# Kernel tuning notes

Measured on AMD Instinct MI355X. Metric: run time of the kernel, lower is better.

## Reference

```python
import jax, jax.numpy as jnp
import numpy as np
from jax import lax

N_LAYERS = 10
N_BLOCKS = 3
N_STACK = N_LAYERS * N_BLOCKS  # 30
WIDTH = 512
SKIP_W = 256
CH = 1
QUANT = 256
BOTTLENECK = 16
KSIZE = 3
SCALE = 2 ** (N_LAYERS - 1)  # 512, nearest upsample factor
B, T = 1, 16384
T_EMB = T // SCALE  # 32


def causal_conv(x, w, b, dilation):
    # x: [B,Cin,T], w: [Cout,Cin,K] -> causal dilated conv, output [B,Cout,T]
    k = w.shape[-1]
    pad = (k - 1) * dilation
    y = lax.conv_general_dilated(x, w, window_strides=(1,), padding=[(pad, 0)],
                                 rhs_dilation=(dilation,),
                                 dimension_numbers=('NCH', 'OIH', 'NCH'))
    return y + b[None, :, None]


def conv1x1(x, w, b):
    # x: [B,Cin,T], w: [Cout,Cin]
    return jnp.einsum('oc,bct->bot', w, x) + b[None, :, None]


def setup_inputs() -> dict:
    key = jax.random.key(0)
    ks = jax.random.split(key, 24)
    s = 0.05
    inp = {
        'x': jax.random.normal(ks[0], (B, CH, T), jnp.float32),
        'embedding': jax.random.normal(ks[1], (B, BOTTLENECK, T_EMB), jnp.float32),
        'w_init': jax.random.normal(ks[2], (WIDTH, CH, KSIZE), jnp.float32) * s,
        'b_init': jnp.zeros((WIDTH,), jnp.float32),
        'w_iskip': jax.random.normal(ks[3], (SKIP_W, WIDTH), jnp.float32) * s,
        'b_iskip': jnp.zeros((SKIP_W,), jnp.float32),
        'w_dil': jax.random.normal(ks[4], (N_STACK, 2 * WIDTH, WIDTH, KSIZE), jnp.float32) * s,
        'b_dil': jnp.zeros((N_STACK, 2 * WIDTH), jnp.float32),
        'w_cond': jax.random.normal(ks[5], (N_STACK, 2 * WIDTH, BOTTLENECK), jnp.float32) * s,
        'b_cond': jnp.zeros((N_STACK, 2 * WIDTH), jnp.float32),
        'w_res': jax.random.normal(ks[6], (N_STACK, WIDTH, WIDTH), jnp.float32) * s,
        'b_res': jnp.zeros((N_STACK, WIDTH), jnp.float32),
        'w_skip': jax.random.normal(ks[7], (N_STACK, SKIP_W, WIDTH), jnp.float32) * s,
        'b_skip': jnp.zeros((N_STACK, SKIP_W), jnp.float32),
        'w_fskip': jax.random.normal(ks[8], (SKIP_W, SKIP_W), jnp.float32) * s,
        'b_fskip': jnp.zeros((SKIP_W,), jnp.float32),
        'w_fcond': jax.random.normal(ks[9], (SKIP_W, BOTTLENECK), jnp.float32) * s,
        'b_fcond': jnp.zeros((SKIP_W,), jnp.float32),
        'w_quant': jax.random.normal(ks[10], (QUANT, SKIP_W), jnp.float32) * s,
        'b_quant': jnp.zeros((QUANT,), jnp.float32),
    }
    return inp


def reference(x, embedding, w_init, b_init, w_iskip, b_iskip, w_dil, b_dil,
              w_cond, b_cond, w_res, b_res, w_skip, b_skip,
              w_fskip, b_fskip, w_fcond, b_fcond, w_quant, b_quant):
    # initial causal conv (kernel 3, dilation 1) + initial skip 1x1
    h = causal_conv(x, w_init, b_init, 1)            # [B,WIDTH,T]
    skip = conv1x1(h, w_iskip, b_iskip)              # [B,SKIP_W,T]
    for i in range(N_STACK):
        dilation = 2 ** (i % N_LAYERS)
        cond = conv1x1(embedding, w_cond[i], b_cond[i])      # [B,2W,T_EMB]
        cond_up = jnp.repeat(cond, SCALE, axis=-1)           # nearest upsample -> [B,2W,T]
        dilated = causal_conv(h, w_dil[i], b_dil[i], dilation) + cond_up
        filters = jax.nn.sigmoid(dilated[:, :WIDTH, :])
        gates = jnp.tanh(dilated[:, WIDTH:, :])
        pre = filters * gates
        h = h + conv1x1(pre, w_res[i], b_res[i])
        skip = skip + conv1x1(pre, w_skip[i], b_skip[i])
    skip = conv1x1(jax.nn.relu(skip), w_fskip, b_fskip)
    fcond = jnp.repeat(conv1x1(embedding, w_fcond, b_fcond), SCALE, axis=-1)
    skip = skip + fcond
    return conv1x1(jax.nn.relu(skip), w_quant, b_quant)     # [B,QUANT,T]
```

## Files before the change

### kernel.cpp

```cpp
#include <hip/hip_runtime.h>


typedef _Float16 f16x8 __attribute__((ext_vector_type(8)));
typedef float f32x4 __attribute__((ext_vector_type(4)));

#define NSTACK 30
#define TLEN   16384

typedef __attribute__((address_space(1))) const unsigned int glob_u32;
typedef __attribute__((address_space(3))) unsigned int lds_u32;

__device__ __forceinline__ void gll16(const unsigned short* g, unsigned short* l) {
  __builtin_amdgcn_global_load_lds((glob_u32*)g, (lds_u32*)l, 16, 0, 0);
}

__device__ __forceinline__ unsigned short f2h(float x) {
  union { _Float16 h; unsigned short u; } c;
  c.h = (_Float16)x;
  return c.u;
}
__device__ __forceinline__ unsigned pack2(float a, float b) {
  return (unsigned)f2h(a) | ((unsigned)f2h(b) << 16);
}
__device__ __forceinline__ float uplo(unsigned u){ union{unsigned v;_Float16 h[2];}c; c.v=u; return (float)c.h[0]; }
__device__ __forceinline__ float uphi(unsigned u){ union{unsigned v;_Float16 h[2];}c; c.v=u; return (float)c.h[1]; }
__device__ __forceinline__ f16x8 ldh(const unsigned short* p) {
  return *(const f16x8*)p;
}
__device__ __forceinline__ float sigmoidf_(float x){ return 1.0f/(1.0f+__expf(-x)); }
__device__ __forceinline__ float tanhf_(float x){ return 1.0f - 2.0f/(__expf(2.0f*x)+1.0f); }
#define MFMA16(a,b,c) __builtin_amdgcn_mfma_f32_16x16x32_f16((a),(b),(c),0,0,0)

#define SEG_T  15728640L
#define SEG_R  1966080L
#define SEG_S  983040L
#define SEG_I  32768L
#define SEG_F  16384L
#define SEG_Q  16384L
#define SEG_C  30976L
#define PREP_TOTAL (SEG_T+SEG_R+SEG_S+SEG_I+SEG_F+SEG_Q+SEG_C)

__device__ __forceinline__ void cast4(const float* src, unsigned short* dst, long g){
  f32x4 v = *(const f32x4*)(src + 4*g);
  unsigned int* d = (unsigned int*)(dst + 4*g);
  d[0] = pack2(v[0], v[1]);
  d[1] = pack2(v[2], v[3]);
}

__global__ void prep_kernel(
    const float* __restrict__ w_dil,  unsigned short* __restrict__ A_dil,
    const float* __restrict__ w_res,  unsigned short* __restrict__ Wres_h,
    const float* __restrict__ w_skip, unsigned short* __restrict__ Wskip_h,
    const float* __restrict__ w_iskip,unsigned short* __restrict__ Wiskip_h,
    const float* __restrict__ w_fskip,unsigned short* __restrict__ Wfskip_h,
    const float* __restrict__ w_quant,unsigned short* __restrict__ Wquant_h,
    const float* __restrict__ emb,
    const float* __restrict__ w_cond, const float* __restrict__ b_cond,
    const float* __restrict__ b_dil,
    const float* __restrict__ w_fcond,const float* __restrict__ b_fcond,
    float* __restrict__ cond_all, float* __restrict__ fcond_all) {
  long g = (long)blockIdx.x*256 + threadIdx.x;
  if (g < SEG_T) {
    int c = (int)(g & 511);
    int m = (int)((g >> 9) & 1023);
    int i = (int)(g >> 19);
    const float* s = w_dil + g*3;
    #pragma unroll
    for (int tap=0; tap<3; ++tap)
      A_dil[(((size_t)i*3+tap)*1024 + m)*512 + c] = f2h(s[tap]);
    return;
  }
  g -= SEG_T;
  if (g < SEG_R) { cast4(w_res,  Wres_h,  g); return; }
  g -= SEG_R;
  if (g < SEG_S) { cast4(w_skip, Wskip_h, g); return; }
  g -= SEG_S;
  if (g < SEG_I) { cast4(w_iskip, Wiskip_h, g); return; }
  g -= SEG_I;
  if (g < SEG_F) { cast4(w_fskip, Wfskip_h, g); return; }
  g -= SEG_F;
  if (g < SEG_Q) { cast4(w_quant, Wquant_h, g); return; }
  g -= SEG_Q;
  if (g < NSTACK*1024) {
    int row = (int)g;
    float acc[32];
    float base = b_cond[row] + b_dil[row];
    #pragma unroll
    for (int e=0;e<32;++e) acc[e] = base;
    #pragma unroll
    for (int c=0;c<16;++c) {
      float wv = w_cond[(size_t)row*16 + c];
      #pragma unroll
      for (int e=0;e<32;++e) acc[e] += wv * emb[c*32+e];
    }
    #pragma unroll
    for (int e=0;e<32;++e) cond_all[(size_t)row*32+e] = acc[e];
  } else if (g < NSTACK*1024 + 256) {
    int m = (int)(g - NSTACK*1024);
    float acc[32];
    float base = b_fcond[m];
    #pragma unroll
    for (int c=0;c<16;++c) {
      float wv = w_fcond[(size_t)m*16 + c];
      #pragma unroll
      for (int e=0;e<32;++e) acc[e] = (c==0 ? base : acc[e]) + wv * emb[c*32+e];
    }
    #pragma unroll
    for (int e=0;e<32;++e) fcond_all[(size_t)m*32+e] = acc[e];
  }
}

__global__ __launch_bounds__(512) void hs_kernel(
    const float* __restrict__ x, const float* __restrict__ w_init,
    const float* __restrict__ b_init,
    unsigned short* __restrict__ h_h16,
    const unsigned short* __restrict__ Wiskip,
    const float* __restrict__ b_iskip, unsigned short* __restrict__ skip16) {
  __shared__ unsigned short S[64][520];
  const int tid = threadIdx.x;
  const int tb = blockIdx.x << 6;

  for (int j = tid; j < 64*128; j += 512) {
    int r  = j >> 7;
    int c4 = (j & 127) << 2;
    int t  = tb + r;
    float xm2 = (t>=2)? x[t-2] : 0.f;
    float xm1 = (t>=1)? x[t-1] : 0.f;
    float x0  = x[t];
    float hv[4];
    #pragma unroll
    for (int q=0;q<4;++q) {
      int cc = c4 + q;
      hv[q] = w_init[cc*3+0]*xm2 + w_init[cc*3+1]*xm1 + w_init[cc*3+2]*x0 + b_init[cc];
    }
    unsigned p0 = pack2(hv[0],hv[1]), p1 = pack2(hv[2],hv[3]);
    unsigned int* hb = (unsigned int*)&h_h16[(size_t)t*512 + c4];
    hb[0] = p0; hb[1] = p1;
    unsigned int* sb = (unsigned int*)&S[r][c4];
    sb[0] = p0; sb[1] = p1;
  }
  __syncthreads();

  const int w = tid >> 6, l = tid & 63, lr = l & 15, lc = l >> 4;
  f32x4 acc[2][4];
  #pragma unroll
  for (int mf=0;mf<2;++mf)
    #pragma unroll
    for (int nf=0;nf<4;++nf) acc[mf][nf] = {0.f,0.f,0.f,0.f};
  for (int kc=0;kc<512;kc+=32) {
    f16x8 b[4];
    #pragma unroll
    for (int nf=0;nf<4;++nf)
      b[nf] = ldh(&S[16*nf+lr][kc + lc*8]);
    #pragma unroll
    for (int mf=0;mf<2;++mf) {
      f16x8 a = ldh(&Wiskip[(size_t)(w*32+16*mf+lr)*512 + kc + lc*8]);
      #pragma unroll
      for (int nf=0;nf<4;++nf)
        acc[mf][nf] = MFMA16(a, b[nf], acc[mf][nf]);
    }
  }
  #pragma unroll
  for (int mf=0;mf<2;++mf)
    #pragma unroll
    for (int nf=0;nf<4;++nf) {
      int s0 = w*32+16*mf+4*lc;
      int t  = tb+16*nf+lr;
      unsigned int* pp = (unsigned int*)&skip16[(size_t)t*256+s0];
      pp[0] = pack2(acc[mf][nf][0]+b_iskip[s0+0], acc[mf][nf][1]+b_iskip[s0+1]);
      pp[1] = pack2(acc[mf][nf][2]+b_iskip[s0+2], acc[mf][nf][3]+b_iskip[s0+3]);
    }
}

__global__ __launch_bounds__(512, 4) void dil_kernel(
    const unsigned short* __restrict__ h_in,
    unsigned short* __restrict__ pre,
    const unsigned short* __restrict__ A_dil,
    const float* __restrict__ cond,
    const unsigned short* __restrict__ zerobuf,
    int dilation) {
  __shared__ unsigned short Ab[2][128][32];
  __shared__ unsigned short Bb[2][256][32];
  const int tid = threadIdx.x;
  const int w = tid >> 6, l = tid & 63;
  const int lr = l & 15, lc = l >> 4;
  const int nt = blockIdx.x & 63, mt = blockIdx.x >> 6;
  const int tb = nt << 8;
  const int e  = tb >> 9;
  const int wr = w >> 2, wc = w & 3;

  const int srowA = (w<<4) + (l>>2);
  const int srowB0 = (w<<5) + (l>>2);
  const int schunk = (l & 3) << 3;

  f32x4 fa[2][4], ga[2][4];
  #pragma unroll
  for (int mf=0;mf<2;++mf)
    #pragma unroll
    for (int nf=0;nf<4;++nf) { fa[mf][nf] = {0.f,0.f,0.f,0.f}; ga[mf][nf] = {0.f,0.f,0.f,0.f}; }

  auto stage = [&](int buf, int s){
    const int tap = s >> 4;
    const int kc  = (s & 15) << 5;
    const int shift = (2 - tap) * dilation;
    {
      const int r = srowA;
      const int m = mt*64 + r + ((r>>6)*448);
      gll16(A_dil + (size_t)tap*(1024*512) + (size_t)m*512 + kc + schunk,
            &Ab[buf][(w<<4)][0]);
    }
    #pragma unroll
    for (int j=0;j<2;++j){
      const int r = srowB0 + (j<<4);
      const int t = tb + r - shift;
      const unsigned short* srcB = (t >= 0) ? (h_in + (size_t)t*512 + kc + schunk)
                                            : (zerobuf + schunk);
      gll16(srcB, &Bb[buf][(w<<5)+(j<<4)][0]);
    }
  };

  stage(0, 0);
  for (int s=0; s<48; ++s) {
    const int cur = s & 1;
    __syncthreads();
    if (s+1 < 48) stage(cur^1, s+1);
    f16x8 af[2], ag[2], bf[4];
    #pragma unroll
    for (int mf=0;mf<2;++mf){
      const int row = (wr<<5) + (mf<<4) + lr;
      af[mf] = ldh(&Ab[cur][row][lc<<3]);
      ag[mf] = ldh(&Ab[cur][64+row][lc<<3]);
    }
    #pragma unroll
    for (int nf=0;nf<4;++nf)
      bf[nf] = ldh(&Bb[cur][(wc<<6)+(nf<<4)+lr][lc<<3]);
    #pragma unroll
    for (int mf=0;mf<2;++mf)
      #pragma unroll
      for (int nf=0;nf<4;++nf){
        fa[mf][nf] = MFMA16(af[mf], bf[nf], fa[mf][nf]);
        ga[mf][nf] = MFMA16(ag[mf], bf[nf], ga[mf][nf]);
      }
  }

  #pragma unroll
  for (int mf=0;mf<2;++mf)
    #pragma unroll
    for (int nf=0;nf<4;++nf){
      const int m0 = mt*64 + (wr<<5) + (mf<<4) + (lc<<2);
      const int t  = tb + (wc<<6) + (nf<<4) + lr;
      float pv[4];
      #pragma unroll
      for (int r=0;r<4;++r){
        float f = fa[mf][nf][r] + cond[(size_t)(m0+r)*32 + e];
        float g = ga[mf][nf][r] + cond[(size_t)(m0+r+512)*32 + e];
        pv[r] = sigmoidf_(f) * tanhf_(g);
      }
      unsigned int* pp = (unsigned int*)&pre[(size_t)t*512 + m0];
      pp[0] = pack2(pv[0], pv[1]);
      pp[1] = pack2(pv[2], pv[3]);
    }
}

__global__ __launch_bounds__(512, 4) void ressk_kernel(
    const unsigned short* __restrict__ pre,
    const unsigned short* __restrict__ h_in,
    unsigned short* __restrict__ h_out,
    unsigned short* __restrict__ skip16,
    const unsigned short* __restrict__ Wres,
    const unsigned short* __restrict__ Wskip,
    const float* __restrict__ b_res,
    const float* __restrict__ b_skip) {
  __shared__ unsigned short Ab[2][128][32];
  __shared__ unsigned short Bb[2][256][32];
  const int tid = threadIdx.x;
  const int w = tid >> 6, l = tid & 63;
  const int lr = l & 15, lc = l >> 4;
  const int nt = blockIdx.x & 63, mt = blockIdx.x >> 6;
  const int tb = nt << 8;
  const int wr = w >> 2, wc = w & 3;
  const bool isres = (mt < 4);
  const unsigned short* W = isres ? Wres : Wskip;
  const int mrow0 = (isres ? mt : (mt-4)) * 128;

  const int srowA = (w<<4) + (l>>2);
  const int srowB0 = (w<<5) + (l>>2);
  const int schunk = (l & 3) << 3;

  f32x4 acc[4][4];
  #pragma unroll
  for (int mf=0;mf<4;++mf)
    #pragma unroll
    for (int nf=0;nf<4;++nf) acc[mf][nf] = {0.f,0.f,0.f,0.f};

  auto stage = [&](int buf, int s){
    const int kc = s << 5;
    gll16(W + (size_t)(mrow0 + srowA)*512 + kc + schunk, &Ab[buf][(w<<4)][0]);
    #pragma unroll
    for (int j=0;j<2;++j){
      const int r = srowB0 + (j<<4);
      gll16(pre + (size_t)(tb + r)*512 + kc + schunk, &Bb[buf][(w<<5)+(j<<4)][0]);
    }
  };

  stage(0, 0);
  for (int s=0; s<16; ++s) {
    const int cur = s & 1;
    __syncthreads();
    if (s+1 < 16) stage(cur^1, s+1);
    f16x8 a[4], bf[4];
    #pragma unroll
    for (int mf=0;mf<4;++mf)
      a[mf] = ldh(&Ab[cur][(wr<<6)+(mf<<4)+lr][lc<<3]);
    #pragma unroll
    for (int nf=0;nf<4;++nf)
      bf[nf] = ldh(&Bb[cur][(wc<<6)+(nf<<4)+lr][lc<<3]);
    #pragma unroll
    for (int mf=0;mf<4;++mf)
      #pragma unroll
      for (int nf=0;nf<4;++nf)
        acc[mf][nf] = MFMA16(a[mf], bf[nf], acc[mf][nf]);
  }

  if (isres) {
    #pragma unroll
    for (int mf=0;mf<4;++mf)
      #pragma unroll
      for (int nf=0;nf<4;++nf){
        const int m0 = mrow0 + (wr<<6) + (mf<<4) + (lc<<2);
        const int t  = tb + (wc<<6) + (nf<<4) + lr;
        const unsigned int* hi = (const unsigned int*)&h_in[(size_t)t*512 + m0];
        unsigned int h01 = hi[0], h23 = hi[1];
        float v0 = uplo(h01) + acc[mf][nf][0] + b_res[m0+0];
        float v1 = uphi(h01) + acc[mf][nf][1] + b_res[m0+1];
        float v2 = uplo(h23) + acc[mf][nf][2] + b_res[m0+2];
        float v3 = uphi(h23) + acc[mf][nf][3] + b_res[m0+3];
        unsigned int* hb = (unsigned int*)&h_out[(size_t)t*512 + m0];
        hb[0] = pack2(v0,v1); hb[1] = pack2(v2,v3);
      }
  } else {
    #pragma unroll
    for (int mf=0;mf<4;++mf)
      #pragma unroll
      for (int nf=0;nf<4;++nf){
        const int s0 = mrow0 + (wr<<6) + (mf<<4) + (lc<<2);
        const int t  = tb + (wc<<6) + (nf<<4) + lr;
        unsigned int* sp = (unsigned int*)&skip16[(size_t)t*256 + s0];
        unsigned int s01 = sp[0], s23 = sp[1];
        float v0 = uplo(s01) + acc[mf][nf][0] + b_skip[s0+0];
        float v1 = uphi(s01) + acc[mf][nf][1] + b_skip[s0+1];
        float v2 = uplo(s23) + acc[mf][nf][2] + b_skip[s0+2];
        float v3 = uphi(s23) + acc[mf][nf][3] + b_skip[s0+3];
        sp[0] = pack2(v0,v1); sp[1] = pack2(v2,v3);
      }
  }
}

__global__ __launch_bounds__(512) void final_kernel(
    const unsigned short* __restrict__ skip16, const unsigned short* __restrict__ Wfs,
    const float* __restrict__ b_fskip, const float* __restrict__ fcond,
    const unsigned short* __restrict__ Wq, const float* __restrict__ b_quant,
    float* __restrict__ out) {
  __shared__ unsigned short S1[64][264];
  __shared__ unsigned short S2[64][264];
  int tid=threadIdx.x, w=tid>>6, l=tid&63, lr=l&15, lc=l>>4;
  int tb = blockIdx.x<<6, e = tb>>9;

  for (int j = tid; j < 64*32; j += 512) {
    int r  = j >> 5;
    int c8 = (j & 31) << 3;
    const unsigned int* sp = (const unsigned int*)&skip16[(size_t)(tb+r)*256 + c8];
    unsigned int* dp = (unsigned int*)&S1[r][c8];
    #pragma unroll
    for (int q=0;q<4;++q){
      unsigned int u = sp[q];
      dp[q] = pack2(fmaxf(uplo(u),0.f), fmaxf(uphi(u),0.f));
    }
  }
  __syncthreads();

  f32x4 acc[2][4];
  #pragma unroll
  for (int mf=0;mf<2;++mf)
    #pragma unroll
    for (int nf=0;nf<4;++nf) acc[mf][nf] = {0.f,0.f,0.f,0.f};
  for (int kc=0;kc<256;kc+=32) {
    f16x8 b[4];
    #pragma unroll
    for (int nf=0;nf<4;++nf) b[nf] = ldh(&S1[16*nf+lr][kc + lc*8]);
    #pragma unroll
    for (int mf=0;mf<2;++mf) {
      f16x8 a = ldh(&Wfs[(size_t)(w*32+16*mf+lr)*256 + kc + lc*8]);
      #pragma unroll
      for (int nf=0;nf<4;++nf)
        acc[mf][nf] = MFMA16(a, b[nf], acc[mf][nf]);
    }
  }
  #pragma unroll
  for (int mf=0;mf<2;++mf)
    #pragma unroll
    for (int nf=0;nf<4;++nf) {
      int m0 = w*32+16*mf+4*lc;
      int n  = 16*nf+lr;
      float pv[4];
      #pragma unroll
      for (int r=0;r<4;++r) {
        float v = acc[mf][nf][r] + b_fskip[m0+r] + fcond[(size_t)(m0+r)*32 + e];
        pv[r] = fmaxf(v, 0.f);
      }
      unsigned int* pp = (unsigned int*)&S2[n][m0];
      pp[0] = pack2(pv[0],pv[1]); pp[1] = pack2(pv[2],pv[3]);
    }
  __syncthreads();

  f32x4 acc2[2][4];
  #pragma unroll
  for (int mf=0;mf<2;++mf)
    #pragma unroll
    for (int nf=0;nf<4;++nf) acc2[mf][nf] = {0.f,0.f,0.f,0.f};
  for (int kc=0;kc<256;kc+=32) {
    f16x8 b[4];
    #pragma unroll
    for (int nf=0;nf<4;++nf) b[nf] = ldh(&S2[16*nf+lr][kc + lc*8]);
    #pragma unroll
    for (int mf=0;mf<2;++mf) {
      f16x8 a = ldh(&Wq[(size_t)(w*32+16*mf+lr)*256 + kc + lc*8]);
      #pragma unroll
      for (int nf=0;nf<4;++nf)
        acc2[mf][nf] = MFMA16(a, b[nf], acc2[mf][nf]);
    }
  }
  #pragma unroll
  for (int mf=0;mf<2;++mf)
    #pragma unroll
    for (int nf=0;nf<4;++nf) {
      int q0 = w*32+16*mf+4*lc;
      int t  = tb + 16*nf + lr;
      #pragma unroll
      for (int r=0;r<4;++r)
        out[(size_t)(q0+r)*TLEN + t] = acc2[mf][nf][r] + b_quant[q0+r];
    }
}


extern "C" void kernel_launch(void* const* d_in, const int* in_sizes, int n_in,
                              void* d_out, int out_size, void* d_ws, size_t ws_size,
                              hipStream_t stream) {
  const float* x       = (const float*)d_in[0];
  const float* emb     = (const float*)d_in[1];
  const float* w_init  = (const float*)d_in[2];
  const float* b_init  = (const float*)d_in[3];
  const float* w_iskip = (const float*)d_in[4];
  const float* b_iskip = (const float*)d_in[5];
  const float* w_dil   = (const float*)d_in[6];
  const float* b_dil   = (const float*)d_in[7];
  const float* w_cond  = (const float*)d_in[8];
  const float* b_cond  = (const float*)d_in[9];
  const float* w_res   = (const float*)d_in[10];
  const float* b_res   = (const float*)d_in[11];
  const float* w_skip  = (const float*)d_in[12];
  const float* b_skip  = (const float*)d_in[13];
  const float* w_fskip = (const float*)d_in[14];
  const float* b_fskip = (const float*)d_in[15];
  const float* w_fcond = (const float*)d_in[16];
  const float* b_fcond = (const float*)d_in[17];
  const float* w_quant = (const float*)d_in[18];
  const float* b_quant = (const float*)d_in[19];
  float* out = (float*)d_out;

  char* ws = (char*)d_ws;
  size_t off = 0;
  auto carve = [&](size_t bytes) -> void* {
    void* p = ws + off;
    off += (bytes + 255) & ~(size_t)255;
    return p;
  };
  unsigned short* A_dil     = (unsigned short*)carve((size_t)NSTACK*3*1024*512*2);
  unsigned short* Wres_h    = (unsigned short*)carve((size_t)NSTACK*512*512*2);
  unsigned short* Wskip_h   = (unsigned short*)carve((size_t)NSTACK*256*512*2);
  unsigned short* Wiskip_h  = (unsigned short*)carve((size_t)256*512*2);
  unsigned short* Wfskip_h  = (unsigned short*)carve((size_t)256*256*2);
  unsigned short* Wquant_h  = (unsigned short*)carve((size_t)256*256*2);
  unsigned short* h_h16     = (unsigned short*)carve((size_t)2*TLEN*512*2);
  unsigned short* pre_h16   = (unsigned short*)carve((size_t)TLEN*512*2);
  unsigned short* skip_h16  = (unsigned short*)carve((size_t)TLEN*256*2);
  float*          cond_all  = (float*)carve((size_t)NSTACK*1024*32*4);
  float*          fcond_all = (float*)carve((size_t)256*32*4);
  unsigned short* zerobuf   = (unsigned short*)carve((size_t)512*2);
  if (off > ws_size) return;

  hipMemsetAsync(zerobuf, 0, 512*2, stream);

  prep_kernel<<<(int)(PREP_TOTAL/256), 256, 0, stream>>>(
      w_dil, A_dil, w_res, Wres_h, w_skip, Wskip_h, w_iskip, Wiskip_h,
      w_fskip, Wfskip_h, w_quant, Wquant_h,
      emb, w_cond, b_cond, b_dil, w_fcond, b_fcond, cond_all, fcond_all);

  hs_kernel<<<TLEN/64, 512, 0, stream>>>(
      x, w_init, b_init, h_h16, Wiskip_h, b_iskip, skip_h16);

  const size_t HB = (size_t)TLEN*512;
  for (int i = 0; i < NSTACK; ++i) {
    int d = 1 << (i % 10);
    const unsigned short* h_in = h_h16 + (size_t)(i & 1)*HB;
    unsigned short* h_out      = h_h16 + (size_t)((i + 1) & 1)*HB;
    dil_kernel<<<512, 512, 0, stream>>>(
        h_in,
        pre_h16,
        A_dil + (size_t)i*3*1024*512,
        cond_all + (size_t)i*1024*32,
        zerobuf,
        d);
    ressk_kernel<<<384, 512, 0, stream>>>(
        pre_h16,
        h_in,
        h_out,
        skip_h16,
        Wres_h + (size_t)i*512*512,
        Wskip_h + (size_t)i*256*512,
        b_res + (size_t)i*512,
        b_skip + (size_t)i*256);
  }

  final_kernel<<<TLEN/64, 512, 0, stream>>>(
      skip_h16, Wfskip_h, b_fskip, fcond_all, Wquant_h, b_quant, out);
}
```

Before: 2.915 ms.

## Add halo-tiled dilated conv kernel reusing one B tile across taps for small dilations

Adds a specialized dilated-conv kernel for dilations up to 64. It stages a single 384-row time window (256 outputs plus a 128-sample causal halo) per K chunk and reads all three taps from it by shifting the LDS row index. This replaces the separate per-tap B loads, cutting global traffic for h. In exchange it uses more LDS per block, and the B buffer is refreshed only every third step, which changes the pipelining cadence.

```diff
diff --git a/kernel.cpp b/kernel.cpp
--- a/kernel.cpp
+++ b/kernel.cpp
@@ -169,6 +169,105 @@
       unsigned int* pp = (unsigned int*)&skip16[(size_t)t*256+s0];
       pp[0] = pack2(acc[mf][nf][0]+b_iskip[s0+0], acc[mf][nf][1]+b_iskip[s0+1]);
       pp[1] = pack2(acc[mf][nf][2]+b_iskip[s0+2], acc[mf][nf][3]+b_iskip[s0+3]);
+    }
+}
+
+__global__ __launch_bounds__(512, 4) void dil_small_kernel(
+    const unsigned short* __restrict__ h_in,
+    unsigned short* __restrict__ pre,
+    const unsigned short* __restrict__ A_dil,
+    const float* __restrict__ cond,
+    const unsigned short* __restrict__ zerobuf,
+    int dilation) {
+  __shared__ unsigned short Ab[2][128][32];
+  __shared__ unsigned short Bb[2][384][32];
+  const int tid = threadIdx.x;
+  const int w = tid >> 6, l = tid & 63;
+  const int lr = l & 15, lc = l >> 4;
+  const int nt = blockIdx.x & 63, mt = blockIdx.x >> 6;
+  const int tb = nt << 8;
+  const int e  = tb >> 9;
+  const int wr = w >> 2, wc = w & 3;
+
+  const int srowA  = (w<<4) + (l>>2);
+  const int srowB0 = w*48 + (l>>2);
+  const int schunk = (l & 3) << 3;
+
+  f32x4 fa[2][4], ga[2][4];
+  #pragma unroll
+  for (int mf=0;mf<2;++mf)
+    #pragma unroll
+    for (int nf=0;nf<4;++nf) { fa[mf][nf] = {0.f,0.f,0.f,0.f}; ga[mf][nf] = {0.f,0.f,0.f,0.f}; }
+
+  auto stageA = [&](int buf, int s){
+    const int kcc = s / 3;
+    const int tap = s - kcc*3;
+    const int kc  = kcc << 5;
+    const int r = srowA;
+    const int m = mt*64 + r + ((r>>6)*448);
+    gll16(A_dil + (size_t)tap*(1024*512) + (size_t)m*512 + kc + schunk,
+          &Ab[buf][(w<<4)][0]);
+  };
+  auto stageB = [&](int buf, int kcc){
+    const int kc = kcc << 5;
+    #pragma unroll
+    for (int j=0;j<3;++j){
+      const int r = srowB0 + j*16;
+      const int t = tb + r - 128;
+      const unsigned short* src = (t >= 0) ? (h_in + (size_t)t*512 + kc + schunk)
+                                           : (zerobuf + schunk);
+      gll16(src, &Bb[buf][w*48 + j*16][0]);
+    }
+  };
+
+  stageA(0, 0);
+  stageB(0, 0);
+  for (int s=0; s<48; ++s) {
+    const int curA = s & 1;
+    const int kcc = s / 3;
+    const int tap = s - kcc*3;
+    const int curB = kcc & 1;
+    __syncthreads();
+    if (s+1 < 48) stageA(curA^1, s+1);
+    if (tap == 2 && kcc+1 < 16) stageB(curB^1, kcc+1);
+    const int shift = (2 - tap) * dilation;
+    f16x8 af[2], ag[2], bf[4];
+    #pragma unroll
+    for (int mf=0;mf<2;++mf){
+      const int row = (wr<<5) + (mf<<4) + lr;
+      af[mf] = ldh(&Ab[curA][row][lc<<3]);
+      ag[mf] = ldh(&Ab[curA][64+row][lc<<3]);
+    }
+    #pragma unroll
+    for (int nf=0;nf<4;++nf){
+      const int col = (wc<<6) + (nf<<4) + lr;
+      bf[nf] = ldh(&Bb[curB][128 + col - shift][lc<<3]);
+    }
+    #pragma unroll
+    for (int mf=0;mf<2;++mf)
+      #pragma unroll
+      for (int nf=0;nf<4;++nf){
+        fa[mf][nf] = MFMA16(af[mf], bf[nf], fa[mf][nf]);
+        ga[mf][nf] = MFMA16(ag[mf], bf[nf], ga[mf][nf]);
+      }
+  }
+
+  #pragma unroll
+  for (int mf=0;mf<2;++mf)
+    #pragma unroll
+    for (int nf=0;nf<4;++nf){
+      const int m0 = mt*64 + (wr<<5) + (mf<<4) + (lc<<2);
+      const int t  = tb + (wc<<6) + (nf<<4) + lr;
+      float pv[4];
+      #pragma unroll
+      for (int r=0;r<4;++r){
+        float f = fa[mf][nf][r] + cond[(size_t)(m0+r)*32 + e];
+        float g = ga[mf][nf][r] + cond[(size_t)(m0+r+512)*32 + e];
+        pv[r] = sigmoidf_(f) * tanhf_(g);
+      }
+      unsigned int* pp = (unsigned int*)&pre[(size_t)t*512 + m0];
+      pp[0] = pack2(pv[0], pv[1]);
+      pp[1] = pack2(pv[2], pv[3]);
     }
 }
 
@@ -504,18 +603,21 @@
     int d = 1 << (i % 10);
     const unsigned short* h_in = h_h16 + (size_t)(i & 1)*HB;
     unsigned short* h_out      = h_h16 + (size_t)((i + 1) & 1)*HB;
-    dil_kernel<<<512, 512, 0, stream>>>(
-        h_in,
-        pre_h16,
-        A_dil + (size_t)i*3*1024*512,
-        cond_all + (size_t)i*1024*32,
-        zerobuf,
-        d);
+    if (d <= 64) {
+      dil_small_kernel<<<512, 512, 0, stream>>>(
+          h_in, pre_h16,
+          A_dil + (size_t)i*3*1024*512,
+          cond_all + (size_t)i*1024*32,
+          zerobuf, d);
+    } else {
+      dil_kernel<<<512, 512, 0, stream>>>(
+          h_in, pre_h16,
+          A_dil + (size_t)i*3*1024*512,
+          cond_all + (size_t)i*1024*32,
+          zerobuf, d);
+    }
     ressk_kernel<<<384, 512, 0, stream>>>(
-        pre_h16,
-        h_in,
-        h_out,
-        skip_h16,
+        pre_h16, h_in, h_out, skip_h16,
         Wres_h + (size_t)i*512*512,
         Wskip_h + (size_t)i*256*512,
         b_res + (size_t)i*512,
```

Result: faster. 2.819 ms (-3.3%).
